# Kernel optimization log

Measured on AMD Instinct MI355X. Metric: run time of the kernel, lower is better.

## Reference

```python
import jax, jax.numpy as jnp
import numpy as np

EPS = 1e-5

def layer_norm(x, g, b):
    m = jnp.mean(x, axis=-1, keepdims=True)
    v = jnp.var(x, axis=-1, keepdims=True)
    return (x - m) / jnp.sqrt(v + EPS) * g + b


def setup_inputs() -> dict:
    key = jax.random.key(0)
    ks = jax.random.split(key, 12)
    B, L, D = 4, 4096, 512
    DF = 2 * D  # dim * dim_ff_scale
    inp = {
        "x": jax.random.normal(ks[0], (B, L, D), dtype=jnp.float32),
        "hidden_real": jax.random.normal(ks[1], (B, D), dtype=jnp.float32),
        "hidden_imag": jax.random.normal(ks[2], (B, D), dtype=jnp.float32),
        # SpiralConv complex params (real/imag parts), as torch.randn cfloat
        "phazor_re": jax.random.normal(ks[3], (D,), dtype=jnp.float32),
        "phazor_im": jax.random.normal(ks[4], (D,), dtype=jnp.float32),
        "pinit_re": jax.random.normal(ks[5], (D,), dtype=jnp.float32),
        "pinit_im": jax.random.normal(ks[6], (D,), dtype=jnp.float32),
        # shared LayerNorm params
        "ln_g": jnp.ones((D,), dtype=jnp.float32),
        "ln_b": jnp.zeros((D,), dtype=jnp.float32),
        # FFN params
        "w1": jax.random.normal(ks[7], (D, DF), dtype=jnp.float32) * (1.0 / np.sqrt(D)),
        "b1": jnp.zeros((DF,), dtype=jnp.float32),
        "w2": jax.random.normal(ks[8], (DF, D), dtype=jnp.float32) * (1.0 / np.sqrt(DF)),
        "b2": jnp.zeros((D,), dtype=jnp.float32),
    }
    return inp


def reference(x, hidden_real, hidden_imag, phazor_re, phazor_im,
              pinit_re, pinit_im, ln_g, ln_b, w1, b1, w2, b2):
    B, L, D = x.shape
    p = jax.lax.complex(phazor_re, phazor_im)
    pinit = jax.lax.complex(pinit_re, pinit_im)
    hidden_last = jax.lax.complex(hidden_real, hidden_imag)

    # phazor = p/|p| * exp(-|p|)  (unit direction, decaying magnitude)
    absp = jnp.abs(p)
    phazor = p / absp * jnp.exp(-absp)

    # phazor_progression[t, d] = phazor[d] ** t
    t = jnp.arange(L, dtype=jnp.float32)
    prog = jnp.exp(t[:, None] * jnp.log(phazor)[None, :])  # [L, D] complex
    filt = prog * pinit[None, :]                            # [L, D]

    x_res = x
    xn = layer_norm(x, ln_g, ln_b)

    # FFT long convolution along sequence, zero-padded to 2L (linear conv)
    filt_fft = jnp.fft.fft(filt, n=2 * L, axis=0)           # [2L, D]
    x_fft = jnp.fft.fft(xn, n=2 * L, axis=1)                # [B, 2L, D]
    conv = jnp.fft.ifft(filt_fft[None, :, :] * x_fft, axis=1)[:, :L, :]

    hidden = conv + hidden_last[:, None, :] * prog[None, :, :] * phazor[None, None, :]

    y = hidden.real + x_res
    yn = layer_norm(y, ln_g, ln_b)
    h = yn @ w1 + b1
    h = h * jax.nn.sigmoid(h)  # SiLU; dropout=0 (eval) is identity
    out = h @ w2 + b2 + y
    return out, hidden
```

## Files before the change

### kernel.cpp

```cpp
#include <hip/hip_runtime.h>
#include <hip/hip_bf16.h>
#include <math.h>

#define BB 4
#define LL 4096
#define DD 512
#define DF 1024
#define CHUNKS 128
#define LC 32
#define HALF_ROWS 8192

typedef __bf16 bf16x8 __attribute__((ext_vector_type(8)));
typedef float f32x4 __attribute__((ext_vector_type(4)));

__device__ inline void get_phazor(const float* __restrict__ pre, const float* __restrict__ pim,
                                  int d, float& ar, float& ai) {
    float pr = pre[d], pi = pim[d];
    float ab = sqrtf(pr * pr + pi * pi);
    float sc = expf(-ab) / ab;
    ar = pr * sc;
    ai = pi * sc;
}

__global__ __launch_bounds__(256) void k_wt(const float* __restrict__ w1, const float* __restrict__ w2,
                                            __bf16* __restrict__ w1t, __bf16* __restrict__ w2t) {
    __shared__ float tile[32][33];
    const float* src;
    __bf16* dst;
    int R, C;
    if (blockIdx.y == 0) { src = w1; dst = w1t; R = DD; C = DF; }
    else                 { src = w2; dst = w2t; R = DF; C = DD; }
    int ntx = C / 32;
    int c0 = (blockIdx.x % ntx) * 32, r0 = (blockIdx.x / ntx) * 32;
    int tx = threadIdx.x & 31, ty = threadIdx.x >> 5;
#pragma unroll
    for (int i = 0; i < 32; i += 8)
        tile[ty + i][tx] = src[(size_t)(r0 + ty + i) * C + c0 + tx];
    __syncthreads();
#pragma unroll
    for (int i = 0; i < 32; i += 8)
        dst[(size_t)(c0 + ty + i) * R + r0 + tx] = (__bf16)tile[tx][ty + i];
}

__global__ __launch_bounds__(512) void k_scan_partial(
    const float* __restrict__ x,
    const float* __restrict__ pre, const float* __restrict__ pim,
    const float* __restrict__ pinr, const float* __restrict__ pini,
    const float* __restrict__ g, const float* __restrict__ bvec,
    float* __restrict__ carry, float* __restrict__ xstats) {
    __shared__ float xt[LC][DD];
    __shared__ float2 st2[LC];
    int d = threadIdx.x;
    int c = blockIdx.x % CHUNKS, b = blockIdx.x / CHUNKS;
    size_t row0 = (size_t)b * LL + (size_t)c * LC;

    const float4* src4 = reinterpret_cast<const float4*>(x + row0 * DD);
    float4* dst4 = reinterpret_cast<float4*>(&xt[0][0]);
#pragma unroll
    for (int j = 0; j < 8; j++) dst4[d + j * 512] = src4[d + j * 512];
    __syncthreads();

    int wv = d >> 6, lane = d & 63;
#pragma unroll
    for (int rr = 0; rr < 4; rr++) {
        int r = wv * 4 + rr;
        float s = 0.f, q = 0.f;
#pragma unroll
        for (int j = 0; j < 8; j++) {
            float v = xt[r][lane + j * 64];
            s += v; q += v * v;
        }
#pragma unroll
        for (int off = 32; off; off >>= 1) { s += __shfl_xor(s, off); q += __shfl_xor(q, off); }
        if (lane == 0) {
            float m = s * (1.0f / DD);
            float rinv = rsqrtf(q * (1.0f / DD) - m * m + 1e-5f);
            st2[r] = make_float2(m, rinv);
            xstats[(row0 + r) * 2 + 0] = m;
            xstats[(row0 + r) * 2 + 1] = rinv;
        }
    }
    __syncthreads();

    float ar, ai;
    get_phazor(pre, pim, d, ar, ai);
    float pr = pinr[d], pi = pini[d];
    float gd = g[d], bd = bvec[d];
    float hr = 0.f, hi = 0.f;
#pragma unroll
    for (int i = 0; i < LC; i++) {
        float2 s2 = st2[i];
        float xn = (xt[i][d] - s2.x) * s2.y * gd + bd;
        float t = ar * hr - ai * hi + pr * xn;
        hi = ar * hi + ai * hr + pi * xn;
        hr = t;
    }
    size_t idx = ((size_t)blockIdx.x * DD + d) * 2;
    carry[idx] = hr;
    carry[idx + 1] = hi;
}

__global__ __launch_bounds__(512) void k_chunk_scan(
    const float* __restrict__ hr0, const float* __restrict__ hi0,
    const float* __restrict__ pre, const float* __restrict__ pim,
    float* __restrict__ carry) {
    int b = blockIdx.x >> 3;
    int dgroup = blockIdx.x & 7;
    int dlocal = threadIdx.x & 63;
    int kt = threadIdx.x >> 6;
    int d = dgroup * 64 + dlocal;
    __shared__ float2 smc[8][64];
    float ar, ai;
    get_phazor(pre, pim, d, ar, ai);
    float Ar = ar, Ai = ai;
#pragma unroll
    for (int p = 1; p < LC; p <<= 1) { float t = Ar * Ar - Ai * Ai; Ai = 2.f * Ar * Ai; Ar = t; }
    float Gr = Ar, Gi = Ai;
#pragma unroll
    for (int p = 0; p < 4; p++) { float t = Gr * Gr - Gi * Gi; Gi = 2.f * Gr * Gi; Gr = t; }
    float2* cp = reinterpret_cast<float2*>(carry);
    size_t base = ((size_t)b * CHUNKS + kt * 16) * DD + d;
    float cr = 0.f, ci = 0.f;
#pragma unroll
    for (int i = 0; i < 16; i++) {
        float2 p2 = cp[base + (size_t)i * DD];
        float t = Ar * cr - Ai * ci + p2.x;
        ci = Ar * ci + Ai * cr + p2.y;
        cr = t;
    }
    smc[kt][dlocal] = make_float2(cr, ci);
    __syncthreads();
    if (kt == 0) {
        float Sr = hr0[b * DD + d], Si = hi0[b * DD + d];
#pragma unroll
        for (int j = 0; j < 8; j++) {
            float2 t2 = smc[j][dlocal];
            smc[j][dlocal] = make_float2(Sr, Si);
            float t = Gr * Sr - Gi * Si + t2.x;
            Si = Gr * Si + Gi * Sr + t2.y;
            Sr = t;
        }
    }
    __syncthreads();
    float2 s0 = smc[kt][dlocal];
    float Sr = s0.x, Si = s0.y;
#pragma unroll
    for (int i = 0; i < 16; i++) {
        float2 p2 = cp[base + (size_t)i * DD];
        cp[base + (size_t)i * DD] = make_float2(Sr, Si);
        float t = Ar * Sr - Ai * Si + p2.x;
        Si = Ar * Si + Ai * Sr + p2.y;
        Sr = t;
    }
}

template <int MODE>
__global__ __launch_bounds__(512) void k_scan_out(
    const float* __restrict__ x, const float* __restrict__ xstats,
    const float* __restrict__ pre, const float* __restrict__ pim,
    const float* __restrict__ pinr, const float* __restrict__ pini,
    const float* __restrict__ g, const float* __restrict__ bvec,
    const float* __restrict__ carry_in,
    float* __restrict__ out_y, float* __restrict__ hid) {
    int d = threadIdx.x;
    int c = blockIdx.x % CHUNKS, b = blockIdx.x / CHUNKS;
    float ar, ai;
    get_phazor(pre, pim, d, ar, ai);
    float pr = pinr[d], pi = pini[d];
    float gd = g[d], bd = bvec[d];
    size_t cidx = ((size_t)blockIdx.x * DD + d) * 2;
    float hr = carry_in[cidx], hi = carry_in[cidx + 1];
    int l0 = c * LC;
    const float* xp = x + ((size_t)b * LL + l0) * DD + d;
    const float* st = xstats + ((size_t)b * LL + l0) * 2;
    for (int i = 0; i < LC; i++) {
        float m = st[2 * i], r = st[2 * i + 1];
        float xv = xp[(size_t)i * DD];
        float xn = (xv - m) * r * gd + bd;
        float ur = pr * xn, ui = pi * xn;
        float t = ar * hr - ai * hi + ur;
        hi = ar * hi + ai * hr + ui;
        hr = t;
        size_t row = (size_t)b * LL + l0 + i;
        if constexpr (MODE == 0) {
            out_y[row * DD + d] = hr + xv;
        } else if constexpr (MODE == 1) {
            hid[row * DD + d] = hr;
        } else if constexpr (MODE == 2) {
            reinterpret_cast<float2*>(hid)[row * DD + d] = make_float2(hr, hi);
        } else {
            out_y[row * DD + d] = hr + xv;
            hid[row * DD + d] = hr;
        }
    }
}

__global__ __launch_bounds__(256) void k_ynorm(const float* __restrict__ y,
                                               const float* __restrict__ g, const float* __restrict__ bvec,
                                               __bf16* __restrict__ yn) {
    int wave = threadIdx.x >> 6, lane = threadIdx.x & 63;
    size_t row = (size_t)blockIdx.x * 4 + wave;
    const float4* yr = reinterpret_cast<const float4*>(y + row * DD) + lane * 2;
    float4 a = yr[0], b = yr[1];
    float s = a.x + a.y + a.z + a.w + b.x + b.y + b.z + b.w;
    float q = a.x * a.x + a.y * a.y + a.z * a.z + a.w * a.w +
              b.x * b.x + b.y * b.y + b.z * b.z + b.w * b.w;
#pragma unroll
    for (int off = 32; off; off >>= 1) {
        s += __shfl_xor(s, off);
        q += __shfl_xor(q, off);
    }
    float m = s * (1.0f / DD);
    float r = rsqrtf(q * (1.0f / DD) - m * m + 1e-5f);
    int dbase = lane * 8;
    const float4* gp = reinterpret_cast<const float4*>(g + dbase);
    const float4* bp = reinterpret_cast<const float4*>(bvec + dbase);
    float4 g0 = gp[0], g1 = gp[1], b0 = bp[0], b1 = bp[1];
    bf16x8 o;
    o[0] = (__bf16)((a.x - m) * r * g0.x + b0.x);
    o[1] = (__bf16)((a.y - m) * r * g0.y + b0.y);
    o[2] = (__bf16)((a.z - m) * r * g0.z + b0.z);
    o[3] = (__bf16)((a.w - m) * r * g0.w + b0.w);
    o[4] = (__bf16)((b.x - m) * r * g1.x + b1.x);
    o[5] = (__bf16)((b.y - m) * r * g1.y + b1.y);
    o[6] = (__bf16)((b.z - m) * r * g1.z + b1.z);
    o[7] = (__bf16)((b.w - m) * r * g1.w + b1.w);
    *reinterpret_cast<bf16x8*>(yn + row * DD + dbase) = o;
}

template <int BM, int BN, int KDIM, int NDIM, int EPI>
__global__ __launch_bounds__(512) void k_gemm(
    const __bf16* __restrict__ A, const __bf16* __restrict__ Bt,
    const float* __restrict__ bias, const float* __restrict__ yadd,
    float* __restrict__ outf, __bf16* __restrict__ outb) {
    __shared__ __align__(16) __bf16 As[2][BM * 64];
    __shared__ __align__(16) __bf16 Bs[2][BN * 64];
    constexpr int NT = NDIM / BN;
    constexpr int MR = BM / 32;
    constexpr int NR = BN / 64;
    constexpr int LPT = BM / 64 + BN / 64;
    int nwg = gridDim.x;
    int bid = blockIdx.x;
    int swz = (bid & 7) * (nwg >> 3) + (bid >> 3);
    int m0 = (swz / NT) * BM;
    int n0 = (swz % NT) * BN;
    int tid = threadIdx.x;
    int wid = tid >> 6, lane = tid & 63;

    f32x4 acc[MR][NR] = {};

    int wm = (wid >> 2) * (BM / 2), wn = (wid & 3) * (BN / 4);
    int fr = lane & 15;
    int qbase = lane >> 4;

    auto stage = [&](int buf, int k0) {
#pragma unroll
        for (int i = 0; i < BM / 64; i++) {
            int c = tid + i * 512;
            int row = c >> 3, kq = c & 7;
            int kqg = kq ^ (row & 7);
            const __bf16* ga = A + (size_t)(m0 + row) * KDIM + k0 + kqg * 8;
            __bf16* la = &As[buf][(size_t)(i * 512 + wid * 64) * 8];
            __builtin_amdgcn_global_load_lds((const __attribute__((address_space(1))) unsigned int*)ga,
                                             (__attribute__((address_space(3))) unsigned int*)la, 16, 0, 0);
        }
#pragma unroll
        for (int i = 0; i < BN / 64; i++) {
            int c = tid + i * 512;
            int row = c >> 3, kq = c & 7;
            int kqg = kq ^ (row & 7);
            const __bf16* gb = Bt + (size_t)(n0 + row) * KDIM + k0 + kqg * 8;
            __bf16* lb = &Bs[buf][(size_t)(i * 512 + wid * 64) * 8];
            __builtin_amdgcn_global_load_lds((const __attribute__((address_space(1))) unsigned int*)gb,
                                             (__attribute__((address_space(3))) unsigned int*)lb, 16, 0, 0);
        }
    };

    auto compute = [&](int buf) {
#pragma unroll
        for (int ks = 0; ks < 2; ks++) {
            int q = ks * 4 + qbase;
            bf16x8 af[MR], bfv[NR];
#pragma unroll
            for (int mi = 0; mi < MR; mi++) {
                int R = wm + mi * 16 + fr;
                af[mi] = *reinterpret_cast<const bf16x8*>(&As[buf][R * 64 + ((q ^ (R & 7)) << 3)]);
            }
#pragma unroll
            for (int ni = 0; ni < NR; ni++) {
                int R = wn + ni * 16 + fr;
                bfv[ni] = *reinterpret_cast<const bf16x8*>(&Bs[buf][R * 64 + ((q ^ (R & 7)) << 3)]);
            }
            __builtin_amdgcn_s_setprio(1);
#pragma unroll
            for (int mi = 0; mi < MR; mi++)
#pragma unroll
                for (int ni = 0; ni < NR; ni++)
                    acc[mi][ni] = __builtin_amdgcn_mfma_f32_16x16x32_bf16(af[mi], bfv[ni],
                                                                          acc[mi][ni], 0, 0, 0);
            __builtin_amdgcn_s_setprio(0);
        }
    };

    stage(0, 0);
    int cur = 0;
    for (int k0 = 64; k0 < KDIM; k0 += 64) {
        stage(cur ^ 1, k0);
        asm volatile("s_waitcnt vmcnt(%0)" ::"i"(LPT) : "memory");
        __builtin_amdgcn_s_barrier();
        compute(cur);
        __builtin_amdgcn_s_barrier();
        cur ^= 1;
    }
    asm volatile("s_waitcnt vmcnt(0)" ::: "memory");
    __builtin_amdgcn_s_barrier();
    compute(cur);

    int orow = (lane >> 4) * 4;
    int ocol = lane & 15;
#pragma unroll
    for (int mi = 0; mi < MR; mi++) {
#pragma unroll
        for (int ni = 0; ni < NR; ni++) {
            int gr = m0 + wm + mi * 16 + orow;
            int gc = n0 + wn + ni * 16 + ocol;
            float bv = bias[gc];
#pragma unroll
            for (int j = 0; j < 4; j++) {
                float v = acc[mi][ni][j] + bv;
                size_t idx = (size_t)(gr + j) * NDIM + gc;
                if constexpr (EPI == 1) {
                    float sv = v / (1.0f + __expf(-v));
                    outb[idx] = (__bf16)sv;
                } else {
                    outf[idx] = v + yadd[idx];
                }
            }
        }
    }
}

extern "C" void kernel_launch(void* const* d_in, const int* in_sizes, int n_in,
                              void* d_out, int out_size, void* d_ws, size_t ws_size,
                              hipStream_t stream) {
    const float* x = (const float*)d_in[0];
    const float* hr0 = (const float*)d_in[1];
    const float* hi0 = (const float*)d_in[2];
    const float* pre = (const float*)d_in[3];
    const float* pim = (const float*)d_in[4];
    const float* pinr = (const float*)d_in[5];
    const float* pini = (const float*)d_in[6];
    const float* lng = (const float*)d_in[7];
    const float* lnb = (const float*)d_in[8];
    const float* w1 = (const float*)d_in[9];
    const float* b1 = (const float*)d_in[10];
    const float* w2 = (const float*)d_in[11];
    const float* b2 = (const float*)d_in[12];

    const size_t n = (size_t)BB * LL * DD;
    const size_t MB1 = 1ull << 20;
    float* outp = (float*)d_out;
    char* hidbase = (char*)d_out + n * 4;
    float* hidp = (float*)hidbase;
    bool interleaved = (out_size >= (int)(3 * n));

    char* ws = (char*)d_ws;
    float* xstats = (float*)ws;      ws += (size_t)BB * LL * 2 * 4;
    float* carry = (float*)ws;       ws += (size_t)BB * CHUNKS * DD * 8;
    __bf16* w1t = (__bf16*)ws;       ws += (size_t)DD * DF * 2;
    __bf16* w2t = (__bf16*)ws;       ws += (size_t)DF * DD * 2;
    char* ws_big = ws;
    const size_t SMALL = ((size_t)128 << 10) + 4 * MB1;
    const size_t NEED_FULL = SMALL + 48 * MB1;
    const size_t NEED_HALF = SMALL + 24 * MB1;

    k_wt<<<dim3((DD / 32) * (DF / 32), 2), 256, 0, stream>>>(w1, w2, w1t, w2t);
    k_scan_partial<<<BB * CHUNKS, 512, 0, stream>>>(x, pre, pim, pinr, pini, lng, lnb,
                                                    carry, xstats);
    k_chunk_scan<<<BB * 8, 512, 0, stream>>>(hr0, hi0, pre, pim, carry);

    if (!interleaved && ws_size >= NEED_FULL) {
        __bf16* yn = (__bf16*)ws_big;
        __bf16* h1 = (__bf16*)(ws_big + 16 * MB1);
        k_scan_out<3><<<BB * CHUNKS, 512, 0, stream>>>(x, xstats, pre, pim, pinr, pini, lng, lnb,
                                                       carry, outp, hidp);
        k_ynorm<<<(BB * LL) / 4, 256, 0, stream>>>(outp, lng, lnb, yn);
        k_gemm<256, 256, DD, DF, 1><<<(BB * LL / 256) * (DF / 256), 512, 0, stream>>>(
            yn, w1t, b1, nullptr, nullptr, h1);
        k_gemm<128, 256, DF, DD, 2><<<(BB * LL / 128) * (DD / 256), 512, 0, stream>>>(
            h1, w2t, b2, outp, outp, nullptr);
    } else if (!interleaved && ws_size >= NEED_HALF) {
        __bf16* yn_h = (__bf16*)ws_big;
        __bf16* h1_h = (__bf16*)(ws_big + 8 * MB1);
        k_scan_out<3><<<BB * CHUNKS, 512, 0, stream>>>(x, xstats, pre, pim, pinr, pini, lng, lnb,
                                                       carry, outp, hidp);
        for (int h = 0; h < 2; h++) {
            float* yh = outp + (size_t)h * HALF_ROWS * DD;
            k_ynorm<<<HALF_ROWS / 4, 256, 0, stream>>>(yh, lng, lnb, yn_h);
            k_gemm<256, 256, DD, DF, 1><<<(HALF_ROWS / 256) * (DF / 256), 512, 0, stream>>>(
                yn_h, w1t, b1, nullptr, nullptr, h1_h);
            k_gemm<128, 256, DF, DD, 2><<<(HALF_ROWS / 128) * (DD / 256), 512, 0, stream>>>(
                h1_h, w2t, b2, yh, yh, nullptr);
        }
    } else {
        __bf16* yn_h = (__bf16*)hidbase;
        __bf16* h1_h = (__bf16*)(hidbase + 8 * MB1);
        k_scan_out<0><<<BB * CHUNKS, 512, 0, stream>>>(x, xstats, pre, pim, pinr, pini, lng, lnb,
                                                       carry, outp, nullptr);
        for (int h = 0; h < 2; h++) {
            float* yh = outp + (size_t)h * HALF_ROWS * DD;
            k_ynorm<<<HALF_ROWS / 4, 256, 0, stream>>>(yh, lng, lnb, yn_h);
            k_gemm<256, 256, DD, DF, 1><<<(HALF_ROWS / 256) * (DF / 256), 512, 0, stream>>>(
                yn_h, w1t, b1, nullptr, nullptr, h1_h);
            k_gemm<128, 256, DF, DD, 2><<<(HALF_ROWS / 128) * (DD / 256), 512, 0, stream>>>(
                h1_h, w2t, b2, yh, yh, nullptr);
        }
        if (interleaved) {
            k_scan_out<2><<<BB * CHUNKS, 512, 0, stream>>>(x, xstats, pre, pim, pinr, pini, lng, lnb,
                                                           carry, nullptr, hidp);
        } else {
            k_scan_out<1><<<BB * CHUNKS, 512, 0, stream>>>(x, xstats, pre, pim, pinr, pini, lng, lnb,
                                                           carry, nullptr, hidp);
        }
    }
}
```

Before: 107.6 us.

## Interleave GEMM global-to-LDS prefetch with MFMA sub-steps using finer waitcnt barriers

Restructures the double-buffered bf16 GEMM main loop: the next tile's A and B loads are split into per-quarter stages interleaved between four compute sub-steps (k-half by m-half). Finer s_waitcnt counts let computing on the first rows start before all of the current tile's loads land. The aim is to hide global-load latency behind MFMA work instead of waiting for a whole stage each iteration. It adds more barriers and depends on exact vmcnt accounting, which is fragile if the load order or counts change. The code also assumes BN/64 == 4, since it always issues four B stages.

```diff
diff --git a/kernel.cpp b/kernel.cpp
--- a/kernel.cpp
+++ b/kernel.cpp
@@ -238,7 +238,9 @@
     constexpr int NT = NDIM / BN;
     constexpr int MR = BM / 32;
     constexpr int NR = BN / 64;
-    constexpr int LPT = BM / 64 + BN / 64;
+    constexpr int MH = MR / 2;
+    constexpr int AQ = BM / 64;
+    constexpr int NKT = KDIM / 64;
     int nwg = gridDim.x;
     int bid = blockIdx.x;
     int swz = (bid & 7) * (nwg >> 3) + (bid >> 3);
@@ -253,68 +255,88 @@
     int fr = lane & 15;
     int qbase = lane >> 4;
 
-    auto stage = [&](int buf, int k0) {
-#pragma unroll
-        for (int i = 0; i < BM / 64; i++) {
-            int c = tid + i * 512;
-            int row = c >> 3, kq = c & 7;
-            int kqg = kq ^ (row & 7);
-            const __bf16* ga = A + (size_t)(m0 + row) * KDIM + k0 + kqg * 8;
-            __bf16* la = &As[buf][(size_t)(i * 512 + wid * 64) * 8];
-            __builtin_amdgcn_global_load_lds((const __attribute__((address_space(1))) unsigned int*)ga,
-                                             (__attribute__((address_space(3))) unsigned int*)la, 16, 0, 0);
-        }
-#pragma unroll
-        for (int i = 0; i < BN / 64; i++) {
-            int c = tid + i * 512;
-            int row = c >> 3, kq = c & 7;
-            int kqg = kq ^ (row & 7);
-            const __bf16* gb = Bt + (size_t)(n0 + row) * KDIM + k0 + kqg * 8;
-            __bf16* lb = &Bs[buf][(size_t)(i * 512 + wid * 64) * 8];
-            __builtin_amdgcn_global_load_lds((const __attribute__((address_space(1))) unsigned int*)gb,
-                                             (__attribute__((address_space(3))) unsigned int*)lb, 16, 0, 0);
-        }
+    auto stageQA = [&](int buf, int k0, int j) {
+        int c = tid + j * 512;
+        int row = c >> 3, kq = c & 7;
+        int kqg = kq ^ (row & 7);
+        const __bf16* ga = A + (size_t)(m0 + row) * KDIM + k0 + kqg * 8;
+        __bf16* la = &As[buf][(size_t)(j * 512 + wid * 64) * 8];
+        __builtin_amdgcn_global_load_lds((const __attribute__((address_space(1))) unsigned int*)ga,
+                                         (__attribute__((address_space(3))) unsigned int*)la, 16, 0, 0);
     };
-
-    auto compute = [&](int buf) {
-#pragma unroll
-        for (int ks = 0; ks < 2; ks++) {
-            int q = ks * 4 + qbase;
-            bf16x8 af[MR], bfv[NR];
-#pragma unroll
-            for (int mi = 0; mi < MR; mi++) {
-                int R = wm + mi * 16 + fr;
-                af[mi] = *reinterpret_cast<const bf16x8*>(&As[buf][R * 64 + ((q ^ (R & 7)) << 3)]);
-            }
-#pragma unroll
-            for (int ni = 0; ni < NR; ni++) {
-                int R = wn + ni * 16 + fr;
-                bfv[ni] = *reinterpret_cast<const bf16x8*>(&Bs[buf][R * 64 + ((q ^ (R & 7)) << 3)]);
-            }
-            __builtin_amdgcn_s_setprio(1);
-#pragma unroll
-            for (int mi = 0; mi < MR; mi++)
-#pragma unroll
-                for (int ni = 0; ni < NR; ni++)
-                    acc[mi][ni] = __builtin_amdgcn_mfma_f32_16x16x32_bf16(af[mi], bfv[ni],
-                                                                          acc[mi][ni], 0, 0, 0);
-            __builtin_amdgcn_s_setprio(0);
-        }
+    auto stageQB = [&](int buf, int k0, int j) {
+        int c = tid + j * 512;
+        int row = c >> 3, kq = c & 7;
+        int kqg = kq ^ (row & 7);
+        const __bf16* gb = Bt + (size_t)(n0 + row) * KDIM + k0 + kqg * 8;
+        __bf16* lb = &Bs[buf][(size_t)(j * 512 + wid * 64) * 8];
+        __builtin_amdgcn_global_load_lds((const __attribute__((address_space(1))) unsigned int*)gb,
+                                         (__attribute__((address_space(3))) unsigned int*)lb, 16, 0, 0);
     };
 
-    stage(0, 0);
-    int cur = 0;
-    for (int k0 = 64; k0 < KDIM; k0 += 64) {
-        stage(cur ^ 1, k0);
-        asm volatile("s_waitcnt vmcnt(%0)" ::"i"(LPT) : "memory");
+    auto quad = [&](int buf, int ks, int mh) {
+        int q = ks * 4 + qbase;
+        bf16x8 af[MH], bfv[NR];
+#pragma unroll
+        for (int mi = 0; mi < MH; mi++) {
+            int R = wm + (mh * MH + mi) * 16 + fr;
+            af[mi] = *reinterpret_cast<const bf16x8*>(&As[buf][R * 64 + ((q ^ (R & 7)) << 3)]);
+        }
+#pragma unroll
+        for (int ni = 0; ni < NR; ni++) {
+            int R = wn + ni * 16 + fr;
+            bfv[ni] = *reinterpret_cast<const bf16x8*>(&Bs[buf][R * 64 + ((q ^ (R & 7)) << 3)]);
+        }
+        __builtin_amdgcn_s_setprio(1);
+#pragma unroll
+        for (int mi = 0; mi < MH; mi++)
+#pragma unroll
+            for (int ni = 0; ni < NR; ni++)
+                acc[mh * MH + mi][ni] = __builtin_amdgcn_mfma_f32_16x16x32_bf16(
+                    af[mi], bfv[ni], acc[mh * MH + mi][ni], 0, 0, 0);
+        __builtin_amdgcn_s_setprio(0);
+    };
+
+    {
+#pragma unroll
+        for (int j = 0; j < 4; j++) stageQB(0, 0, j);
+        if constexpr (AQ == 4) { stageQA(0, 0, 0); stageQA(0, 0, 2); stageQA(0, 0, 1); stageQA(0, 0, 3); }
+        else                   { stageQA(0, 0, 0); stageQA(0, 0, 1); }
+    }
+
+    for (int t = 0; t < NKT; t++) {
+        int buf = t & 1;
+        int k1 = (t + 1) * 64;
+        bool pre = (t + 1 < NKT);
         __builtin_amdgcn_s_barrier();
-        compute(cur);
+        if (pre) { stageQB(buf ^ 1, k1, 0); stageQB(buf ^ 1, k1, 1); }
+        if constexpr (AQ == 4) {
+            if (pre) asm volatile("s_waitcnt vmcnt(4)" ::: "memory");
+            else     asm volatile("s_waitcnt vmcnt(2)" ::: "memory");
+        } else {
+            if (pre) asm volatile("s_waitcnt vmcnt(2)" ::: "memory");
+            else     asm volatile("s_waitcnt vmcnt(0)" ::: "memory");
+        }
         __builtin_amdgcn_s_barrier();
-        cur ^= 1;
-    }
-    asm volatile("s_waitcnt vmcnt(0)" ::: "memory");
-    __builtin_amdgcn_s_barrier();
-    compute(cur);
+        quad(buf, 0, 0);
+        if (pre) { stageQB(buf ^ 1, k1, 2); stageQB(buf ^ 1, k1, 3); }
+        if constexpr (AQ == 4) {
+            if (pre) asm volatile("s_waitcnt vmcnt(4)" ::: "memory");
+            else     asm volatile("s_waitcnt vmcnt(0)" ::: "memory");
+            __builtin_amdgcn_s_barrier();
+        }
+        quad(buf, 0, 1);
+        if (pre) {
+            if constexpr (AQ == 4) { stageQA(buf ^ 1, k1, 0); stageQA(buf ^ 1, k1, 2); }
+            else                   { stageQA(buf ^ 1, k1, 0); }
+        }
+        quad(buf, 1, 0);
+        if (pre) {
+            if constexpr (AQ == 4) { stageQA(buf ^ 1, k1, 1); stageQA(buf ^ 1, k1, 3); }
+            else                   { stageQA(buf ^ 1, k1, 1); }
+        }
+        quad(buf, 1, 1);
+    }
 
     int orow = (lane >> 4) * 4;
     int ocol = lane & 15;
```

Result: slower. 116.3 us (+8.1%).
